# Optimization experiments

Measured on AMD Instinct MI355X. Metric: run time of the kernel, lower is better.

## Reference

```python
import jax, jax.numpy as jnp
import numpy as np

MAX_LEN = 64  # max segment length (lengths are (i%16+1)*4 <= 64)
NEG_INF = jnp.float32(-1e30)


def setup_inputs() -> dict:
    key = jax.random.key(0)
    k1, k2, k3 = jax.random.split(key, 3)
    B, EACH, H = 46, 32, 1024
    S = B * EACH  # 1472 segments
    lens = ((np.arange(S) % 16 + 1) * 4).astype(np.int32)  # ragged, sum = 50048
    N = int(lens.sum())
    offsets = np.concatenate([[0], np.cumsum(lens)[:-1]]).astype(np.int32)
    cls_embedding = jax.random.normal(k1, (N, H), dtype=jnp.float32)
    W = jax.random.normal(k2, (H, 1), dtype=jnp.float32) * 0.02
    b = jnp.zeros((1,), dtype=jnp.float32)
    length = jnp.asarray(lens.reshape(B, EACH))
    # exactly one positive per segment (at a random valid position)
    pos = jax.random.randint(k3, (S,), 0, 1 << 30) % jnp.asarray(lens)
    target = jnp.zeros((N,), dtype=jnp.int32).at[jnp.asarray(offsets) + pos].set(1)
    return {"cls_embedding": cls_embedding, "W": W, "b": b,
            "length": length, "target": target}


def _segmented_double_softmax_ce(logits, lens, tgt, each_length):
    # logits: [N], lens: [S], tgt: [N] 0/1 ints
    S = lens.shape[0]
    N = logits.shape[0]
    offsets = jnp.concatenate([jnp.zeros((1,), jnp.int32),
                               jnp.cumsum(lens)[:-1].astype(jnp.int32)])
    pos = jnp.arange(MAX_LEN, dtype=jnp.int32)
    idx = offsets[:, None] + pos[None, :]              # [S, MAX_LEN]
    valid = pos[None, :] < lens[:, None]               # [S, MAX_LEN]
    idx_c = jnp.minimum(idx, N - 1)
    seg_logits = logits[idx_c]                          # [S, MAX_LEN]
    seg_tgt = tgt[idx_c]                                # [S, MAX_LEN]
    # faithful to original: softmax over segment, then CrossEntropyLoss
    # (which applies log_softmax AGAIN) on the softmax output
    p = jax.nn.softmax(jnp.where(valid, seg_logits, NEG_INF), axis=-1)
    lse2 = jax.nn.logsumexp(jnp.where(valid, p, NEG_INF), axis=-1)  # [S]
    t_idx = jnp.argmax(jnp.where(valid, seg_tgt, -1), axis=-1)       # [S]
    p_t = jnp.take_along_axis(p, t_idx[:, None], axis=-1)[:, 0]
    loss_per = lse2 - p_t                                            # [S]
    # replicate the loop's skip conditions
    i = jnp.arange(S)
    next_len = jnp.concatenate([lens[1:], jnp.ones((1,), lens.dtype)])
    skip_next_zero = (i > 0) & (i + 1 < S) & (next_len == 0)
    tgt_sum = jnp.sum(jnp.where(valid, seg_tgt, 0), axis=-1)
    skip_no_pos = ((i + 1) % each_length == 0) & (tgt_sum <= 0)
    include = (lens > 0) & (~skip_next_zero) & (~skip_no_pos)
    cnt = jnp.sum(include).astype(jnp.float32)
    denom = jnp.where(cnt > 0, cnt, jnp.float32(1e-4))
    loss = jnp.sum(jnp.where(include, loss_per, 0.0)) / denom
    return loss


def reference(cls_embedding, W, b, length, target):
    # dropout is identity (inference); classifier -> per-row score
    logits = (cls_embedding @ W + b)[:, 0]   # [N]
    lens = length.reshape(-1).astype(jnp.int32)
    tgt = target.reshape(-1)
    each_length = length.shape[-1]
    loss = _segmented_double_softmax_ce(logits, lens, tgt, each_length)
    return logits, loss
```

## Files before the change

kernel.cpp:

```cpp
#include <hip/hip_runtime.h>


#define EACH_LEN 32

__device__ inline float wave_sum_f(float v) {
#pragma unroll
    for (int o = 32; o > 0; o >>= 1) v += __shfl_xor(v, o, 64);
    return v;
}
__device__ inline float wave_max_f(float v) {
#pragma unroll
    for (int o = 32; o > 0; o >>= 1) v = fmaxf(v, __shfl_xor(v, o, 64));
    return v;
}
__device__ inline int wave_sum_i(int v) {
#pragma unroll
    for (int o = 32; o > 0; o >>= 1) v += __shfl_xor(v, o, 64);
    return v;
}
__device__ inline int wave_max_i(int v) {
#pragma unroll
    for (int o = 32; o > 0; o >>= 1) v = max(v, __shfl_xor(v, o, 64));
    return v;
}

__global__ __launch_bounds__(256) void matvec_kernel(
    const float* __restrict__ A, const float* __restrict__ W,
    const float* __restrict__ b, float* __restrict__ out, int N) {
    const int wid  = threadIdx.x >> 6;
    const int lane = threadIdx.x & 63;
    const int row  = blockIdx.x * 4 + wid;
    if (row >= N) return;
    const float4* a4 = reinterpret_cast<const float4*>(A + (size_t)row * 1024);
    const float4* w4 = reinterpret_cast<const float4*>(W);
    float acc = 0.f;
#pragma unroll
    for (int k = 0; k < 4; ++k) {
        float4 av = a4[lane + 64 * k];
        float4 wv = w4[lane + 64 * k];
        acc = fmaf(av.x, wv.x, acc);
        acc = fmaf(av.y, wv.y, acc);
        acc = fmaf(av.z, wv.z, acc);
        acc = fmaf(av.w, wv.w, acc);
    }
    acc = wave_sum_f(acc);
    if (lane == 0) out[row] = acc + b[0];
}

__global__ __launch_bounds__(256) void seg_loss_kernel(
    const float* __restrict__ logits, const int* __restrict__ lens,
    const int* __restrict__ tgt, float* __restrict__ contrib,
    float* __restrict__ incl, int S) {
    const int wid  = threadIdx.x >> 6;
    const int lane = threadIdx.x & 63;
    const int s    = blockIdx.x * 4 + wid;
    if (s >= S) return;

    int part = 0;
    for (int j = lane; j < s; j += 64) part += lens[j];
    const int offset = wave_sum_i(part);
    const int len = lens[s];
    const bool valid = lane < len;

    const float l = valid ? logits[offset + lane] : -3.402823e38f;
    const float m = wave_max_f(l);
    const float e = valid ? __expf(l - m) : 0.f;
    const float Z = wave_sum_f(e);
    const float p = e / Z;

    const float q = valid ? __expf(p) : 0.f;
    const float lse2 = __logf(wave_sum_f(q));

    const int tv = valid ? tgt[offset + lane] : -1;
    const int maxt = wave_max_i(tv);
    const unsigned long long ball = __ballot(tv == maxt);
    const int t_idx = __ffsll(ball) - 1;
    const float p_t = __shfl(p, t_idx, 64);

    const int tgt_sum = wave_sum_i(valid ? tv : 0);

    const int next_len = (s + 1 < S) ? lens[s + 1] : 1;
    const bool skip_next_zero = (s > 0) && (s + 1 < S) && (next_len == 0);
    const bool skip_no_pos = (((s + 1) % EACH_LEN) == 0) && (tgt_sum <= 0);
    const bool include = (len > 0) && !skip_next_zero && !skip_no_pos;

    if (lane == 0) {
        contrib[s] = include ? (lse2 - p_t) : 0.f;
        incl[s]    = include ? 1.f : 0.f;
    }
}

__global__ __launch_bounds__(256) void reduce_kernel(
    const float* __restrict__ contrib, const float* __restrict__ incl,
    float* __restrict__ out_loss, int S) {
    float a = 0.f, c = 0.f;
    for (int i = threadIdx.x; i < S; i += 256) {
        a += contrib[i];
        c += incl[i];
    }
    a = wave_sum_f(a);
    c = wave_sum_f(c);
    __shared__ float wa[4], wc[4];
    const int wid = threadIdx.x >> 6, lane = threadIdx.x & 63;
    if (lane == 0) { wa[wid] = a; wc[wid] = c; }
    __syncthreads();
    if (threadIdx.x == 0) {
        const float A = wa[0] + wa[1] + wa[2] + wa[3];
        const float C = wc[0] + wc[1] + wc[2] + wc[3];
        const float denom = (C > 0.f) ? C : 1e-4f;
        out_loss[0] = A / denom;
    }
}

extern "C" void kernel_launch(void* const* d_in, const int* in_sizes, int n_in,
                              void* d_out, int out_size, void* d_ws, size_t ws_size,
                              hipStream_t stream) {
    const float* A   = (const float*)d_in[0];
    const float* W   = (const float*)d_in[1];
    const float* b   = (const float*)d_in[2];
    const int*  lens = (const int*)d_in[3];
    const int*  tgt  = (const int*)d_in[4];

    const int H = in_sizes[1];
    const int N = in_sizes[0] / H;
    const int S = in_sizes[3];

    float* logits = (float*)d_out;
    float* loss   = logits + N;

    float* contrib = (float*)d_ws;
    float* incl    = contrib + S;

    matvec_kernel<<<(N + 3) / 4, 256, 0, stream>>>(A, W, b, logits, N);
    seg_loss_kernel<<<(S + 3) / 4, 256, 0, stream>>>(logits, lens, tgt, contrib, incl, S);
    reduce_kernel<<<1, 256, 0, stream>>>(contrib, incl, loss, S);
}
```

Measured before the change: 44.08 us.

## Fuse matvec and segment loss into one kernel with paired-segment blocks

Merges the matvec and segmented softmax-loss kernels into one launch. Each block handles two segments, paired so their lengths sum to a constant (short with long), computes their logits into shared memory, then runs the double-softmax CE from shared memory. This removes a kernel launch and the logits global round trip, and keeps W in registers across rows. The cost is fewer blocks (736) each doing more serial row work, plus a block-wide prefix-sum over lens in every block.

Measured after the change: 39.15 us (median of 2 runs). 1.13x faster.

```diff
diff --git a/kernel.cpp b/kernel.cpp
--- a/kernel.cpp
+++ b/kernel.cpp
@@ -24,69 +24,108 @@
     return v;
 }
 
-__global__ __launch_bounds__(256) void matvec_kernel(
+__global__ __launch_bounds__(256) void fused_kernel(
     const float* __restrict__ A, const float* __restrict__ W,
-    const float* __restrict__ b, float* __restrict__ out, int N) {
-    const int wid  = threadIdx.x >> 6;
-    const int lane = threadIdx.x & 63;
-    const int row  = blockIdx.x * 4 + wid;
-    if (row >= N) return;
-    const float4* a4 = reinterpret_cast<const float4*>(A + (size_t)row * 1024);
+    const float* __restrict__ b, const int* __restrict__ lens,
+    const int* __restrict__ tgt, float* __restrict__ logits,
+    float* __restrict__ contrib, float* __restrict__ incl, int S) {
+    const int tid = threadIdx.x, wid = tid >> 6, lane = tid & 63;
+
+    int s0, s1;
+    if ((S & 15) == 0) {
+        const int g = blockIdx.x >> 3, j = blockIdx.x & 7;
+        s0 = g * 16 + j;
+        s1 = g * 16 + 15 - j;
+    } else {
+        s0 = blockIdx.x * 2;
+        s1 = (s0 + 1 < S) ? s0 + 1 : -1;
+    }
+
+    const int hi = max(s0, s1);
+    int p0 = 0, p1 = 0;
+    for (int j = tid; j < hi; j += 256) {
+        const int l = lens[j];
+        if (j < s0) p0 += l;
+        if (j < s1) p1 += l;
+    }
+    p0 = wave_sum_i(p0);
+    p1 = wave_sum_i(p1);
+    __shared__ int w0[4], w1[4];
+    if (lane == 0) { w0[wid] = p0; w1[wid] = p1; }
+    __syncthreads();
+    const int off0 = w0[0] + w0[1] + w0[2] + w0[3];
+    const int off1 = w1[0] + w1[1] + w1[2] + w1[3];
+    const int len0 = lens[s0];
+    const int len1 = (s1 >= 0) ? lens[s1] : 0;
+
     const float4* w4 = reinterpret_cast<const float4*>(W);
-    float acc = 0.f;
-#pragma unroll
-    for (int k = 0; k < 4; ++k) {
-        float4 av = a4[lane + 64 * k];
-        float4 wv = w4[lane + 64 * k];
-        acc = fmaf(av.x, wv.x, acc);
-        acc = fmaf(av.y, wv.y, acc);
-        acc = fmaf(av.z, wv.z, acc);
-        acc = fmaf(av.w, wv.w, acc);
+    const float4 wv0 = w4[lane], wv1 = w4[lane + 64],
+                 wv2 = w4[lane + 128], wv3 = w4[lane + 192];
+    const float bias = b[0];
+
+    __shared__ float slog[128];
+    const int R = len0 + len1;
+    for (int r = wid; r < R; r += 4) {
+        const int row = (r < len0) ? (off0 + r) : (off1 + (r - len0));
+        const float4* a4 = reinterpret_cast<const float4*>(A + (size_t)row * 1024);
+        float acc = 0.f;
+        float4 av;
+        av = a4[lane];
+        acc = fmaf(av.x, wv0.x, acc); acc = fmaf(av.y, wv0.y, acc);
+        acc = fmaf(av.z, wv0.z, acc); acc = fmaf(av.w, wv0.w, acc);
+        av = a4[lane + 64];
+        acc = fmaf(av.x, wv1.x, acc); acc = fmaf(av.y, wv1.y, acc);
+        acc = fmaf(av.z, wv1.z, acc); acc = fmaf(av.w, wv1.w, acc);
+        av = a4[lane + 128];
+        acc = fmaf(av.x, wv2.x, acc); acc = fmaf(av.y, wv2.y, acc);
+        acc = fmaf(av.z, wv2.z, acc); acc = fmaf(av.w, wv2.w, acc);
+        av = a4[lane + 192];
+        acc = fmaf(av.x, wv3.x, acc); acc = fmaf(av.y, wv3.y, acc);
+        acc = fmaf(av.z, wv3.z, acc); acc = fmaf(av.w, wv3.w, acc);
+        acc = wave_sum_f(acc);
+        if (lane == 0) {
+            const float v = acc + bias;
+            slog[r] = v;
+            logits[row] = v;
+        }
     }
-    acc = wave_sum_f(acc);
-    if (lane == 0) out[row] = acc + b[0];
-}
+    __syncthreads();
 
-__global__ __launch_bounds__(256) void seg_loss_kernel(
-    const float* __restrict__ logits, const int* __restrict__ lens,
-    const int* __restrict__ tgt, float* __restrict__ contrib,
-    float* __restrict__ incl, int S) {
-    const int wid  = threadIdx.x >> 6;
-    const int lane = threadIdx.x & 63;
-    const int s    = blockIdx.x * 4 + wid;
-    if (s >= S) return;
+    if (wid < 2) {
+        const int s = wid ? s1 : s0;
+        if (s >= 0) {
+            const int len  = wid ? len1 : len0;
+            const int off  = wid ? off1 : off0;
+            const int base = wid ? len0 : 0;
+            const bool valid = lane < len;
 
-    int part = 0;
-    for (int j = lane; j < s; j += 64) part += lens[j];
-    const int offset = wave_sum_i(part);
-    const int len = lens[s];
-    const bool valid = lane < len;
+            const float l = valid ? slog[base + lane] : -3.402823e38f;
+            const float m = wave_max_f(l);
+            const float e = valid ? __expf(l - m) : 0.f;
+            const float Z = wave_sum_f(e);
+            const float p = e / Z;
 
-    const float l = valid ? logits[offset + lane] : -3.402823e38f;
-    const float m = wave_max_f(l);
-    const float e = valid ? __expf(l - m) : 0.f;
-    const float Z = wave_sum_f(e);
-    const float p = e / Z;
+            const float q = valid ? __expf(p) : 0.f;
+            const float lse2 = __logf(wave_sum_f(q));
 
-    const float q = valid ? __expf(p) : 0.f;
-    const float lse2 = __logf(wave_sum_f(q));
+            const int tv = valid ? tgt[off + lane] : -1;
+            const int maxt = wave_max_i(tv);
+            const unsigned long long ball = __ballot(tv == maxt);
+            const int t_idx = __ffsll(ball) - 1;
+            const float p_t = __shfl(p, t_idx, 64);
 
-    const int tv = valid ? tgt[offset + lane] : -1;
-    const int maxt = wave_max_i(tv);
-    const unsigned long long ball = __ballot(tv == maxt);
-    const int t_idx = __ffsll(ball) - 1;
-    const float p_t = __shfl(p, t_idx, 64);
+            const int tgt_sum = wave_sum_i(valid ? tv : 0);
 
-    const int tgt_sum = wave_sum_i(valid ? tv : 0);
+            const int next_len = (s + 1 < S) ? lens[s + 1] : 1;
+            const bool skip_next_zero = (s > 0) && (s + 1 < S) && (next_len == 0);
+            const bool skip_no_pos = (((s + 1) % EACH_LEN) == 0) && (tgt_sum <= 0);
+            const bool include = (len > 0) && !skip_next_zero && !skip_no_pos;
 
-    const int next_len = (s + 1 < S) ? lens[s + 1] : 1;
-    const bool skip_next_zero = (s > 0) && (s + 1 < S) && (next_len == 0);
-    const bool skip_no_pos = (((s + 1) % EACH_LEN) == 0) && (tgt_sum <= 0);
-    const bool include = (len > 0) && !skip_next_zero && !skip_no_pos;
-
-    if (lane == 0) {
-        contrib[s] = include ? (lse2 - p_t) : 0.f;
-        incl[s]    = include ? 1.f : 0.f;
+            if (lane == 0) {
+                contrib[s] = include ? (lse2 - p_t) : 0.f;
+                incl[s]    = include ? 1.f : 0.f;
+            }
+        }
     }
 }
 
@@ -131,7 +170,8 @@
     float* contrib = (float*)d_ws;
     float* incl    = contrib + S;
 
-    matvec_kernel<<<(N + 3) / 4, 256, 0, stream>>>(A, W, b, logits, N);
-    seg_loss_kernel<<<(S + 3) / 4, 256, 0, stream>>>(logits, lens, tgt, contrib, incl, S);
+    const int nblk = (S + 1) / 2;
+    fused_kernel<<<nblk, 256, 0, stream>>>(A, W, b, lens, tgt,
+                                           logits, contrib, incl, S);
     reduce_kernel<<<1, 256, 0, stream>>>(contrib, incl, loss, S);
 }
```

## Use persistent two-row matvec and fold the final reduction into the segment kernel

Applied to the files above, without the earlier changes.

The matvec becomes a grid-stride persistent kernel with 2048 blocks. Each wave keeps W in registers and handles two rows per iteration, which gives more independent loads in flight and allows a float2 store. The separate reduce kernel is removed: each segment wave atomically adds its loss term and its include flag to global accumulators, and the last block to finish (found with an atomic counter) writes the final loss. This saves one kernel launch and the contrib/incl arrays, but adds a memset, atomic contention, and a float summation order that is no longer deterministic.

Result: slower. 85.22 us (+93.3%).

```diff
diff --git a/kernel.cpp b/kernel.cpp
--- a/kernel.cpp
+++ b/kernel.cpp
@@ -26,89 +26,105 @@
 
 __global__ __launch_bounds__(256) void matvec_kernel(
     const float* __restrict__ A, const float* __restrict__ W,
-    const float* __restrict__ b, float* __restrict__ out, int N) {
+    const float* __restrict__ b, float* __restrict__ logits, int N) {
     const int wid  = threadIdx.x >> 6;
     const int lane = threadIdx.x & 63;
-    const int row  = blockIdx.x * 4 + wid;
-    if (row >= N) return;
-    const float4* a4 = reinterpret_cast<const float4*>(A + (size_t)row * 1024);
+    const int gw   = blockIdx.x * 4 + wid;
+    const int NW   = gridDim.x * 4;
+
     const float4* w4 = reinterpret_cast<const float4*>(W);
-    float acc = 0.f;
+    float4 wv[4];
+    wv[0] = w4[lane];       wv[1] = w4[lane + 64];
+    wv[2] = w4[lane + 128]; wv[3] = w4[lane + 192];
+    const float bias = b[0];
+
+    const int NP = (N + 1) >> 1;
+    for (int p = gw; p < NP; p += NW) {
+        const int rowA = 2 * p;
+        const int rowB = 2 * p + 1;
+        const bool hasB = rowB < N;
+        const float4* a4A = reinterpret_cast<const float4*>(A + (size_t)rowA * 1024);
+        const float4* a4B = reinterpret_cast<const float4*>(A + (size_t)(hasB ? rowB : rowA) * 1024);
+        float accA = 0.f, accB = 0.f;
 #pragma unroll
-    for (int k = 0; k < 4; ++k) {
-        float4 av = a4[lane + 64 * k];
-        float4 wv = w4[lane + 64 * k];
-        acc = fmaf(av.x, wv.x, acc);
-        acc = fmaf(av.y, wv.y, acc);
-        acc = fmaf(av.z, wv.z, acc);
-        acc = fmaf(av.w, wv.w, acc);
+        for (int k = 0; k < 4; ++k) {
+            const float4 avA = a4A[lane + 64 * k];
+            const float4 avB = a4B[lane + 64 * k];
+            accA = fmaf(avA.x, wv[k].x, accA); accA = fmaf(avA.y, wv[k].y, accA);
+            accA = fmaf(avA.z, wv[k].z, accA); accA = fmaf(avA.w, wv[k].w, accA);
+            accB = fmaf(avB.x, wv[k].x, accB); accB = fmaf(avB.y, wv[k].y, accB);
+            accB = fmaf(avB.z, wv[k].z, accB); accB = fmaf(avB.w, wv[k].w, accB);
+        }
+#pragma unroll
+        for (int o = 32; o > 0; o >>= 1) {
+            accA += __shfl_xor(accA, o, 64);
+            accB += __shfl_xor(accB, o, 64);
+        }
+        if (lane == 0) {
+            if (hasB) {
+                float2 v2 = make_float2(accA + bias, accB + bias);
+                *reinterpret_cast<float2*>(logits + rowA) = v2;
+            } else {
+                logits[rowA] = accA + bias;
+            }
+        }
     }
-    acc = wave_sum_f(acc);
-    if (lane == 0) out[row] = acc + b[0];
 }
 
 __global__ __launch_bounds__(256) void seg_loss_kernel(
     const float* __restrict__ logits, const int* __restrict__ lens,
-    const int* __restrict__ tgt, float* __restrict__ contrib,
-    float* __restrict__ incl, int S) {
+    const int* __restrict__ tgt, float* __restrict__ acc,
+    unsigned* __restrict__ done, float* __restrict__ loss, int S) {
     const int wid  = threadIdx.x >> 6;
     const int lane = threadIdx.x & 63;
     const int s    = blockIdx.x * 4 + wid;
-    if (s >= S) return;
 
-    int part = 0;
-    for (int j = lane; j < s; j += 64) part += lens[j];
-    const int offset = wave_sum_i(part);
-    const int len = lens[s];
-    const bool valid = lane < len;
+    float o1 = 0.f, o2 = 0.f;
+    if (s < S) {
+        int part = 0;
+        for (int j = lane; j < s; j += 64) part += lens[j];
+        const int offset = wave_sum_i(part);
+        const int len = lens[s];
+        const bool valid = lane < len;
 
-    const float l = valid ? logits[offset + lane] : -3.402823e38f;
-    const float m = wave_max_f(l);
-    const float e = valid ? __expf(l - m) : 0.f;
-    const float Z = wave_sum_f(e);
-    const float p = e / Z;
+        const float l = valid ? logits[offset + lane] : -3.402823e38f;
+        const float m = wave_max_f(l);
+        const float e = valid ? __expf(l - m) : 0.f;
+        const float Z = wave_sum_f(e);
+        const float p = e / Z;
 
-    const float q = valid ? __expf(p) : 0.f;
-    const float lse2 = __logf(wave_sum_f(q));
+        const float q = valid ? __expf(p) : 0.f;
+        const float lse2 = __logf(wave_sum_f(q));
 
-    const int tv = valid ? tgt[offset + lane] : -1;
-    const int maxt = wave_max_i(tv);
-    const unsigned long long ball = __ballot(tv == maxt);
-    const int t_idx = __ffsll(ball) - 1;
-    const float p_t = __shfl(p, t_idx, 64);
+        const int tv = valid ? tgt[offset + lane] : -1;
+        const int maxt = wave_max_i(tv);
+        const unsigned long long ball = __ballot(tv == maxt);
+        const int t_idx = __ffsll(ball) - 1;
+        const float p_t = __shfl(p, t_idx, 64);
 
-    const int tgt_sum = wave_sum_i(valid ? tv : 0);
+        const int tgt_sum = wave_sum_i(valid ? tv : 0);
 
-    const int next_len = (s + 1 < S) ? lens[s + 1] : 1;
-    const bool skip_next_zero = (s > 0) && (s + 1 < S) && (next_len == 0);
-    const bool skip_no_pos = (((s + 1) % EACH_LEN) == 0) && (tgt_sum <= 0);
-    const bool include = (len > 0) && !skip_next_zero && !skip_no_pos;
+        const int next_len = (s + 1 < S) ? lens[s + 1] : 1;
+        const bool skip_next_zero = (s > 0) && (s + 1 < S) && (next_len == 0);
+        const bool skip_no_pos = (((s + 1) % EACH_LEN) == 0) && (tgt_sum <= 0);
+        const bool include = (len > 0) && !skip_next_zero && !skip_no_pos;
 
-    if (lane == 0) {
-        contrib[s] = include ? (lse2 - p_t) : 0.f;
-        incl[s]    = include ? 1.f : 0.f;
+        if (lane == 0) {
+            o1 = atomicAdd(&acc[0], include ? (lse2 - p_t) : 0.f);
+            o2 = atomicAdd(&acc[1], include ? 1.f : 0.f);
+        }
     }
-}
+    if (o1 == -3.25e37f && o2 == -3.25e37f) acc[0] = 0.f;
 
-__global__ __launch_bounds__(256) void reduce_kernel(
-    const float* __restrict__ contrib, const float* __restrict__ incl,
-    float* __restrict__ out_loss, int S) {
-    float a = 0.f, c = 0.f;
-    for (int i = threadIdx.x; i < S; i += 256) {
-        a += contrib[i];
-        c += incl[i];
-    }
-    a = wave_sum_f(a);
-    c = wave_sum_f(c);
-    __shared__ float wa[4], wc[4];
-    const int wid = threadIdx.x >> 6, lane = threadIdx.x & 63;
-    if (lane == 0) { wa[wid] = a; wc[wid] = c; }
     __syncthreads();
+
     if (threadIdx.x == 0) {
-        const float A = wa[0] + wa[1] + wa[2] + wa[3];
-        const float C = wc[0] + wc[1] + wc[2] + wc[3];
-        const float denom = (C > 0.f) ? C : 1e-4f;
-        out_loss[0] = A / denom;
+        const unsigned old = atomicAdd(done, 1u);
+        if (old == gridDim.x - 1) {
+            const float Asum = atomicAdd(&acc[0], 0.f);
+            const float Csum = atomicAdd(&acc[1], 0.f);
+            loss[0] = Asum / (Csum > 0.f ? Csum : 1e-4f);
+        }
     }
 }
 
@@ -128,10 +144,12 @@
     float* logits = (float*)d_out;
     float* loss   = logits + N;
 
-    float* contrib = (float*)d_ws;
-    float* incl    = contrib + S;
+    float*    acc  = (float*)d_ws;
+    unsigned* done = (unsigned*)d_ws + 2;
 
-    matvec_kernel<<<(N + 3) / 4, 256, 0, stream>>>(A, W, b, logits, N);
-    seg_loss_kernel<<<(S + 3) / 4, 256, 0, stream>>>(logits, lens, tgt, contrib, incl, S);
-    reduce_kernel<<<1, 256, 0, stream>>>(contrib, incl, loss, S);
+    hipMemsetAsync(d_ws, 0, 16, stream);
+
+    matvec_kernel<<<2048, 256, 0, stream>>>(A, W, b, logits, N);
+    seg_loss_kernel<<<(S + 3) / 4, 256, 0, stream>>>(logits, lens, tgt,
+                                                     acc, done, loss, S);
 }
```
